# Kernel optimization log

Hardware: AMD Instinct MI355X
Metric: run time of the kernel (lower is better)

## Reference

```python
import jax, jax.numpy as jnp
import numpy as np

B, T, F, NL = 2048, 128, 256, 7      # batch, num_trees, num_feature, n_layers
N = 2 ** NL - 1                       # 127 nodes per perfect tree
L = 2 ** (NL - 1)                     # 64 leaves per tree


def setup_inputs() -> dict:
    key = jax.random.key(0)
    k1, k2, k3, k4 = jax.random.split(key, 4)
    x = jax.random.normal(k1, (B, F), dtype=jnp.float32)
    # One-hot split-feature selector per node (faithful to the ctor's weight rows)
    split_idx = jax.random.randint(k2, (T, N), 0, F)
    weights = jax.nn.one_hot(split_idx, F, dtype=jnp.float32)      # [T, N, F]
    biases = jax.random.normal(k3, (T, N), dtype=jnp.float32)      # split thresholds
    leaves = jax.random.normal(k4, (T, L), dtype=jnp.float32) * 0.1
    base_score = jnp.array([0.5], dtype=jnp.float32)
    return {"x": x, "weights": weights, "biases": biases, "leaves": leaves,
            "base_score": base_score, "n_layers": NL}


def reference(x, weights, biases, leaves, base_score, n_layers):
    # Eval-mode forward (self.training == False): hard heaviside routing.
    b, t = x.shape[0], weights.shape[0]
    # F.linear(input, weights, -biases) for all trees at once: [B, T, N]
    cond = jnp.einsum('bf,tnf->btn', x, weights) - biases[None]
    # torch.heaviside(v, 0): 1 if v > 0 else 0 (0 at v == 0)
    act = (cond > 0).astype(x.dtype)
    acts = jnp.stack([1.0 - act, act], axis=-1)                    # [B, T, N, 2]
    # Root layer: out = acts[:, 0, :] per tree -> [B, T, 2, 1]
    out = acts[:, :, 0, :].reshape(b, t, 2, 1)
    # Layer-by-layer path-probability product down the perfect tree
    for l in range(1, n_layers - 1):
        curr = acts[:, :, 2 ** l - 1: 2 ** (l + 1) - 1, :]         # [B, T, 2^l, 2]
        out = (curr * out).reshape(b, t, -1, 1)
    out = out.reshape(b, t, -1) * leaves[None]                     # [B, T, L]
    preds = jnp.sum(out, axis=-1)                                  # per-tree pred [B, T]
    return jnp.sum(preds, axis=-1) + base_score                    # [B]
```

## Files before the change

kernel.cpp:

```cpp
#include <hip/hip_runtime.h>

constexpr int B  = 2048;
constexpr int T  = 128;
constexpr int F  = 256;
constexpr int N  = 127;
constexpr int NU = 63;
constexpr int L  = 64;

__global__ __launch_bounds__(256) void extract_kernel(const float4* __restrict__ w4,
                                                      const float* __restrict__ biases,
                                                      int2* __restrict__ nodes) {
    const int i = blockIdx.x * 256 + threadIdx.x;
    const float4 v = w4[i];
#pragma unroll
    for (int j = 0; j < 4; ++j) {
        const float val = (j == 0) ? v.x : (j == 1) ? v.y : (j == 2) ? v.z : v.w;
        if (val > 0.5f) {
            const int e = i * 4 + j;
            const int f = e & (F - 1);
            const int g = e >> 8;
            const int t = g / N;
            const int n = g - t * N;
            if (n < NU) {
                int2 rec;
                rec.x = f;
                rec.y = __float_as_int(biases[g]);
                nodes[n * T + t] = rec;
            }
        }
    }
}

__global__ __launch_bounds__(128) void traverse_kernel(const float* __restrict__ x,
                                                       const float* __restrict__ leaves,
                                                       const float* __restrict__ base,
                                                       const int2* __restrict__ nodes,
                                                       float* __restrict__ out) {
    const int b = blockIdx.x;
    const int t = threadIdx.x;

    __shared__ float xs[F];
    reinterpret_cast<float2*>(xs)[t] =
        reinterpret_cast<const float2*>(x + (size_t)b * F)[t];
    __syncthreads();

    int idx = 0;
#pragma unroll
    for (int l = 0; l < 6; ++l) {
        const int2  nd = nodes[idx * T + t];
        const float c  = xs[nd.x] - __int_as_float(nd.y);
        idx = 2 * idx + 1 + (c > 0.0f ? 1 : 0);
    }
    float pred = leaves[t * L + (idx - NU)];

#pragma unroll
    for (int off = 32; off > 0; off >>= 1)
        pred += __shfl_down(pred, off, 64);

    __shared__ float wsum[2];
    if ((t & 63) == 0) wsum[t >> 6] = pred;
    __syncthreads();
    if (t == 0) out[b] = wsum[0] + wsum[1] + base[0];
}

extern "C" void kernel_launch(void* const* d_in, const int* in_sizes, int n_in,
                              void* d_out, int out_size, void* d_ws, size_t ws_size,
                              hipStream_t stream) {
    const float* x       = (const float*)d_in[0];
    const float* weights = (const float*)d_in[1];
    const float* biases  = (const float*)d_in[2];
    const float* leaves  = (const float*)d_in[3];
    const float* base    = (const float*)d_in[4];
    float* out = (float*)d_out;

    int2* nodes = (int2*)d_ws;

    extract_kernel<<<(T * N * F / 4) / 256, 256, 0, stream>>>(
        (const float4*)weights, biases, nodes);
    traverse_kernel<<<B, 128, 0, stream>>>(x, leaves, base, nodes, out);
}
```

Measured before the change: 78.87 us.

## Skip leaf-level weight rows in extraction and prefetch both child nodes

The extract kernel now launches only over the 63 internal nodes per tree, so it no longer reads the one-hot weight rows for the 64 leaf-level nodes that were previously discarded. This roughly halves the weight traffic. The traverse kernel speculatively loads both children of the current node before evaluating the comparison, which takes the global load off the dependent critical path of each level. It issues twice the node loads per level in exchange.

```diff
diff --git a/kernel.cpp b/kernel.cpp
--- a/kernel.cpp
+++ b/kernel.cpp
@@ -11,22 +11,19 @@
                                                       const float* __restrict__ biases,
                                                       int2* __restrict__ nodes) {
     const int i = blockIdx.x * 256 + threadIdx.x;
-    const float4 v = w4[i];
+    const int r = i >> 6;
+    const int c = i & 63;
+    const int t = r / NU;
+    const int n = r - t * NU;
+    const float4 v = w4[((size_t)t * N + n) * (F / 4) + c];
 #pragma unroll
     for (int j = 0; j < 4; ++j) {
         const float val = (j == 0) ? v.x : (j == 1) ? v.y : (j == 2) ? v.z : v.w;
         if (val > 0.5f) {
-            const int e = i * 4 + j;
-            const int f = e & (F - 1);
-            const int g = e >> 8;
-            const int t = g / N;
-            const int n = g - t * N;
-            if (n < NU) {
-                int2 rec;
-                rec.x = f;
-                rec.y = __float_as_int(biases[g]);
-                nodes[n * T + t] = rec;
-            }
+            int2 rec;
+            rec.x = c * 4 + j;
+            rec.y = __float_as_int(biases[t * N + n]);
+            nodes[n * T + t] = rec;
         }
     }
 }
@@ -45,12 +42,17 @@
     __syncthreads();
 
     int idx = 0;
+    int2 nd = nodes[t];
 #pragma unroll
-    for (int l = 0; l < 6; ++l) {
-        const int2  nd = nodes[idx * T + t];
-        const float c  = xs[nd.x] - __int_as_float(nd.y);
-        idx = 2 * idx + 1 + (c > 0.0f ? 1 : 0);
+    for (int l = 0; l < 5; ++l) {
+        const int2 cl = nodes[(2 * idx + 1) * T + t];
+        const int2 cr = nodes[(2 * idx + 2) * T + t];
+        const bool right = xs[nd.x] > __int_as_float(nd.y);
+        idx = 2 * idx + 1 + (right ? 1 : 0);
+        nd = right ? cr : cl;
     }
+    const bool right = xs[nd.x] > __int_as_float(nd.y);
+    idx = 2 * idx + 1 + (right ? 1 : 0);
     float pred = leaves[t * L + (idx - NU)];
 
 #pragma unroll
@@ -75,7 +77,7 @@
 
     int2* nodes = (int2*)d_ws;
 
-    extract_kernel<<<(T * N * F / 4) / 256, 256, 0, stream>>>(
+    extract_kernel<<<(T * NU * (F / 4)) / 256, 256, 0, stream>>>(
         (const float4*)weights, biases, nodes);
     traverse_kernel<<<B, 128, 0, stream>>>(x, leaves, base, nodes, out);
 }
```

After: 78.74 us. No clear change (-0.2%).
